# Optimization experiments

Hardware: AMD Instinct MI355X
Metric: run time of the kernel (lower is better)

The kernel has to match this reference:

```python
import jax, jax.numpy as jnp
import numpy as np

VOCAB, HIDDEN, EMBED = 30522, 768, 512
PAD_INDEX = 0
NEG_SLOPE = 0.1


def setup_inputs() -> dict:
    key = jax.random.key(0)
    k1, k2, k3, k4 = jax.random.split(key, 4)
    words = jax.random.randint(k1, (16, 512, 4), 0, VOCAB, dtype=jnp.int64) if jax.config.jax_enable_x64 else jax.random.randint(k1, (16, 512, 4), 0, VOCAB, dtype=jnp.int32)
    embed_table = jax.random.normal(k2, (VOCAB, HIDDEN), dtype=jnp.float32) * 0.02
    w_ffn = jax.random.normal(k3, (HIDDEN, EMBED), dtype=jnp.float32) * 0.02
    b_ffn = jax.random.normal(k4, (EMBED,), dtype=jnp.float32) * 0.02
    return {"words": words, "embed_table": embed_table, "w_ffn": w_ffn, "b_ffn": b_ffn}


def reference(words, embed_table, w_ffn, b_ffn):
    # words: [B, S, W] subword ids; pad_index marks padding subwords/words.
    B, S, W = words.shape
    sub_mask = words != PAD_INDEX                      # [B,S,W] valid subwords
    word_valid = jnp.any(sub_mask, axis=-1)            # [B,S]  words with >=1 subword
    lens = jnp.sum(word_valid, axis=-1)                # [B]    valid words per sequence

    # Stub of transformer last_hidden_state: per-token hidden vectors. [B,S,W,H]
    x = embed_table[words]

    # Masked mean over subwords of each word (segment mean-pool).
    m = sub_mask[..., None].astype(x.dtype)
    cnt = jnp.maximum(jnp.sum(sub_mask, axis=-1), 1)[..., None].astype(x.dtype)
    pooled = jnp.sum(x * m, axis=2) / cnt              # [B,S,H]

    # pad = x[0, -1] of flattened [B, S*W, H] == hidden of last flat token of batch 0
    pad_vec = x[0, -1, -1]                             # [H]

    # Stable compaction: valid words first (mirrors pop-in-order + pad append).
    order = jnp.argsort(jnp.logical_not(word_valid), axis=1, stable=True)  # [B,S]
    pooled_c = jnp.take_along_axis(pooled, order[..., None], axis=1)       # [B,S,H]
    keep = (jnp.arange(S)[None, :] < lens[:, None])[..., None]             # [B,S,1]
    x_seq = jnp.where(keep, pooled_c, pad_vec)         # [B,S,H]

    # FFN: Linear + LeakyReLU(0.1)
    return jax.nn.leaky_relu(x_seq @ w_ffn + b_ffn, NEG_SLOPE)
```

## Files before the change

### kernel.cpp

```cpp
#include <hip/hip_runtime.h>
#include <stdint.h>

#define HIDDEN 768
#define EMBED  512
#define BATCH  16
#define SEQ    512
#define NWORDS (BATCH*SEQ)
#define PAD_FLAT_IDX 2047
#define NEG_SLOPE 0.1f
#define NPOOLBLK 2048

__device__ __forceinline__ unsigned short f2bf(float f) {
    unsigned int x = __float_as_uint(f);
    unsigned int r = x + 0x7fffu + ((x >> 16) & 1u);
    return (unsigned short)(r >> 16);
}

__global__ __launch_bounds__(256) void combo_kernel(const int* __restrict__ words,
                                                    const float* __restrict__ w,
                                                    const float* __restrict__ table,
                                                    unsigned short* __restrict__ xseq,
                                                    unsigned short* __restrict__ wt) {
    if (blockIdx.x < NPOOLBLK) {
        __shared__ unsigned long long mask[8];
        int b    = blockIdx.x >> 7;
        int wave = threadIdx.x >> 6;
        int lane = threadIdx.x & 63;

        int p0 = wave * 64 + lane;
        int p1 = p0 + 256;
        int4 wa = ((const int4*)words)[b * SEQ + p0];
        int4 wb = ((const int4*)words)[b * SEQ + p1];
        unsigned long long mlo = __ballot((wa.x | wa.y | wa.z | wa.w) != 0);
        unsigned long long mhi = __ballot((wb.x | wb.y | wb.z | wb.w) != 0);
        if (lane == 0) { mask[wave] = mlo; mask[4 + wave] = mhi; }
        __syncthreads();

        int s = (blockIdx.x & 127) * 4 + wave;
        int seg = s >> 6;
        int bit = s & 63;
        int vp = 0, tot = 0;
#pragma unroll
        for (int i = 0; i < 8; ++i) {
            unsigned long long m = mask[i];
            int c = __popcll(m);
            if (i < seg) vp += c;
            tot += c;
        }
        unsigned long long mseg = mask[seg];
        vp += __popcll(mseg & ((1ull << bit) - 1ull));
        bool valid = (mseg >> bit) & 1ull;
        int d = valid ? vp : (tot + (s - vp));
        int drow = b * SEQ + d;

        int4 w4 = ((const int4*)words)[b * SEQ + s];
        int cnt = (w4.x != 0) + (w4.y != 0) + (w4.z != 0) + (w4.w != 0);

        float sx[3] = {0.f, 0.f, 0.f}, sy[3] = {0.f, 0.f, 0.f};
        float sz[3] = {0.f, 0.f, 0.f}, sw[3] = {0.f, 0.f, 0.f};
        if (cnt == 0) {
            int pid = words[PAD_FLAT_IDX];
            const float4* rp = (const float4*)(table + (size_t)pid * HIDDEN);
#pragma unroll
            for (int c = 0; c < 3; ++c) {
                float4 v = rp[lane + 64 * c];
                sx[c] = v.x; sy[c] = v.y; sz[c] = v.z; sw[c] = v.w;
            }
            cnt = 1;
        } else {
            int id[4] = {w4.x, w4.y, w4.z, w4.w};
#pragma unroll
            for (int j = 0; j < 4; ++j) {
                if (id[j] != 0) {
                    const float4* rp = (const float4*)(table + (size_t)id[j] * HIDDEN);
#pragma unroll
                    for (int c = 0; c < 3; ++c) {
                        float4 v = rp[lane + 64 * c];
                        sx[c] += v.x; sy[c] += v.y; sz[c] += v.z; sw[c] += v.w;
                    }
                }
            }
        }
        float inv = 1.0f / (float)cnt;
#pragma unroll
        for (int c = 0; c < 3; ++c) {
            ushort4 o;
            o.x = f2bf(sx[c] * inv); o.y = f2bf(sy[c] * inv);
            o.z = f2bf(sz[c] * inv); o.w = f2bf(sw[c] * inv);
            *(ushort4*)&xseq[(size_t)drow * HIDDEN + (lane + 64 * c) * 4] = o;
        }
    } else {
        __shared__ float tile[32][33];
        int bid = blockIdx.x - NPOOLBLK;
        int k0 = (bid % (HIDDEN / 32)) * 32;
        int n0 = (bid / (HIDDEN / 32)) * 32;
        int tc = threadIdx.x & 31;
        int tr = threadIdx.x >> 5;
#pragma unroll
        for (int i = 0; i < 4; ++i) {
            int r = tr + i * 8;
            tile[r][tc] = w[(size_t)(k0 + r) * EMBED + n0 + tc];
        }
        __syncthreads();
#pragma unroll
        for (int i = 0; i < 4; ++i) {
            int r = tr + i * 8;
            wt[(size_t)(n0 + r) * HIDDEN + k0 + tc] = f2bf(tile[tc][r]);
        }
    }
}

typedef __attribute__((ext_vector_type(8))) short bf16x8;
typedef __attribute__((ext_vector_type(4))) float f32x4;

__device__ __forceinline__ void load_lds16(const void* g, void* l) {
    __builtin_amdgcn_global_load_lds(
        (const __attribute__((address_space(1))) unsigned int*)g,
        (__attribute__((address_space(3))) unsigned int*)l,
        16, 0, 0);
}

#define BM 128
#define BN 64
#define BK 32
#define NSTEP (HIDDEN / BK)
#define NBUF 4

__global__ __launch_bounds__(256) void gemm_kernel(const unsigned short* __restrict__ A,
                                                   const unsigned short* __restrict__ Bt,
                                                   const float* __restrict__ bias,
                                                   float* __restrict__ out) {
    __shared__ unsigned short sA[NBUF][BM * BK];
    __shared__ unsigned short sB[NBUF][BN * BK];

    int tid = threadIdx.x;
    int bid = blockIdx.x;
    int swz = (bid & 7) * 64 + (bid >> 3);
    int m0  = (swz >> 3) * BM;
    int n0  = (swz & 7) * BN;
    int wave = tid >> 6;
    int lane = tid & 63;
    int wr   = wave >> 1;
    int wc   = wave & 1;
    int quad = lane >> 4;
    int l16  = lane & 15;

    f32x4 acc[4][2] = {};

    const unsigned short* ga0 = A  + (size_t)(m0 + (tid >> 2)) * HIDDEN + (tid & 3) * 8;
    const unsigned short* ga1 = A  + (size_t)(m0 + 64 + (tid >> 2)) * HIDDEN + (tid & 3) * 8;
    const unsigned short* gb  = Bt + (size_t)(n0 + (tid >> 2)) * HIDDEN + (tid & 3) * 8;

    load_lds16(ga0,      &sA[0][tid * 8]);
    load_lds16(ga1,      &sA[0][(256 + tid) * 8]);
    load_lds16(gb,       &sB[0][tid * 8]);
    load_lds16(ga0 + BK, &sA[1][tid * 8]);
    load_lds16(ga1 + BK, &sA[1][(256 + tid) * 8]);
    load_lds16(gb  + BK, &sB[1][tid * 8]);

#pragma unroll
    for (int t = 0; t < NSTEP; ++t) {
        if (t + 2 < NSTEP) {
            const int k0  = (t + 2) * BK;
            const int buf = (t + 2) & (NBUF - 1);
            load_lds16(ga0 + k0, &sA[buf][tid * 8]);
            load_lds16(ga1 + k0, &sA[buf][(256 + tid) * 8]);
            load_lds16(gb  + k0, &sB[buf][tid * 8]);
        }
        if (t < NSTEP - 2)
            asm volatile("s_waitcnt vmcnt(6)\n\ts_barrier" ::: "memory");
        else if (t == NSTEP - 2)
            asm volatile("s_waitcnt vmcnt(3)\n\ts_barrier" ::: "memory");
        else
            asm volatile("s_waitcnt vmcnt(0)\n\ts_barrier" ::: "memory");

        const int buf = t & (NBUF - 1);
        bf16x8 af[4], bfr[2];
#pragma unroll
        for (int mt = 0; mt < 4; ++mt)
            af[mt] = *(const bf16x8*)&sA[buf][(wr * 64 + mt * 16 + l16) * BK + quad * 8];
#pragma unroll
        for (int nt = 0; nt < 2; ++nt)
            bfr[nt] = *(const bf16x8*)&sB[buf][(wc * 32 + nt * 16 + l16) * BK + quad * 8];

#pragma unroll
        for (int mt = 0; mt < 4; ++mt)
#pragma unroll
            for (int nt = 0; nt < 2; ++nt)
                acc[mt][nt] = __builtin_amdgcn_mfma_f32_16x16x32_bf16(
                    af[mt], bfr[nt], acc[mt][nt], 0, 0, 0);
    }

#pragma unroll
    for (int nt = 0; nt < 2; ++nt) {
        int col = n0 + wc * 32 + nt * 16 + l16;
        float bv = bias[col];
#pragma unroll
        for (int mt = 0; mt < 4; ++mt) {
            int rbase = m0 + wr * 64 + mt * 16 + quad * 4;
#pragma unroll
            for (int r = 0; r < 4; ++r) {
                float v = acc[mt][nt][r] + bv;
                v = (v > 0.f) ? v : v * NEG_SLOPE;
                out[(size_t)(rbase + r) * EMBED + col] = v;
            }
        }
    }
}

extern "C" void kernel_launch(void* const* d_in, const int* in_sizes, int n_in,
                              void* d_out, int out_size, void* d_ws, size_t ws_size,
                              hipStream_t stream) {
    (void)in_sizes; (void)n_in; (void)out_size; (void)ws_size;
    const int*   words = (const int*)d_in[0];
    const float* table = (const float*)d_in[1];
    const float* wffn  = (const float*)d_in[2];
    const float* bffn  = (const float*)d_in[3];
    float* out = (float*)d_out;

    char* ws = (char*)d_ws;
    unsigned short* xseq = (unsigned short*)ws;
    unsigned short* wt   = (unsigned short*)(ws + 12582912);

    combo_kernel<<<NPOOLBLK + (HIDDEN / 32) * (EMBED / 32), 256, 0, stream>>>(
        words, wffn, table, xseq, wt);
    gemm_kernel<<<NWORDS / BM * (EMBED / BN), 256, 0, stream>>>(xseq, wt, bffn, out);
}
```

Baseline: 160.6 us.

## Fuse pooling, weight transpose and GEMM into one persistent kernel with grid barrier

```diff
diff --git a/kernel.cpp b/kernel.cpp
--- a/kernel.cpp
+++ b/kernel.cpp
@@ -8,7 +8,11 @@
 #define NWORDS (BATCH*SEQ)
 #define PAD_FLAT_IDX 2047
 #define NEG_SLOPE 0.1f
-#define NPOOLBLK 2048
+
+#define NBLK       512
+#define XSEQ_BYTES 12582912
+#define WT_BYTES   786432
+#define CTR_OFF    (XSEQ_BYTES + WT_BYTES)
 
 __device__ __forceinline__ unsigned short f2bf(float f) {
     unsigned int x = __float_as_uint(f);
@@ -16,19 +20,41 @@
     return (unsigned short)(r >> 16);
 }
 
-__global__ __launch_bounds__(256) void combo_kernel(const int* __restrict__ words,
-                                                    const float* __restrict__ w,
-                                                    const float* __restrict__ table,
-                                                    unsigned short* __restrict__ xseq,
-                                                    unsigned short* __restrict__ wt) {
-    if (blockIdx.x < NPOOLBLK) {
-        __shared__ unsigned long long mask[8];
-        int b    = blockIdx.x >> 7;
-        int wave = threadIdx.x >> 6;
-        int lane = threadIdx.x & 63;
-
-        int p0 = wave * 64 + lane;
-        int p1 = p0 + 256;
+typedef __attribute__((ext_vector_type(8))) short bf16x8;
+typedef __attribute__((ext_vector_type(4))) float f32x4;
+
+__device__ __forceinline__ void load_lds16(const void* g, void* l) {
+    __builtin_amdgcn_global_load_lds(
+        (const __attribute__((address_space(1))) unsigned int*)g,
+        (__attribute__((address_space(3))) unsigned int*)l,
+        16, 0, 0);
+}
+
+#define BM 128
+#define BN 64
+#define BK 32
+#define NSTEP (HIDDEN / BK)
+#define NBUF 4
+
+__global__ __launch_bounds__(256, 2) void fused_kernel(
+    const int* __restrict__ words, const float* __restrict__ w,
+    const float* __restrict__ table, const float* __restrict__ bias,
+    float* __restrict__ out, unsigned short* __restrict__ xseq,
+    unsigned short* __restrict__ wt, unsigned int* __restrict__ ctr)
+{
+    __shared__ unsigned short sA[NBUF][BM * BK];
+    __shared__ unsigned short sB[NBUF][BN * BK];
+    __shared__ unsigned long long mask[8];
+
+    int tid  = threadIdx.x;
+    int bid  = blockIdx.x;
+    int wave = tid >> 6;
+    int lane = tid & 63;
+
+    {
+        int b = bid >> 5;
+        int q = bid & 31;
+        int p0 = wave * 64 + lane, p1 = p0 + 256;
         int4 wa = ((const int4*)words)[b * SEQ + p0];
         int4 wb = ((const int4*)words)[b * SEQ + p1];
         unsigned long long mlo = __ballot((wa.x | wa.y | wa.z | wa.w) != 0);
@@ -36,66 +62,86 @@
         if (lane == 0) { mask[wave] = mlo; mask[4 + wave] = mhi; }
         __syncthreads();
 
-        int s = (blockIdx.x & 127) * 4 + wave;
-        int seg = s >> 6;
-        int bit = s & 63;
-        int vp = 0, tot = 0;
-#pragma unroll
-        for (int i = 0; i < 8; ++i) {
-            unsigned long long m = mask[i];
-            int c = __popcll(m);
-            if (i < seg) vp += c;
-            tot += c;
-        }
-        unsigned long long mseg = mask[seg];
-        vp += __popcll(mseg & ((1ull << bit) - 1ull));
-        bool valid = (mseg >> bit) & 1ull;
-        int d = valid ? vp : (tot + (s - vp));
-        int drow = b * SEQ + d;
-
-        int4 w4 = ((const int4*)words)[b * SEQ + s];
-        int cnt = (w4.x != 0) + (w4.y != 0) + (w4.z != 0) + (w4.w != 0);
-
-        float sx[3] = {0.f, 0.f, 0.f}, sy[3] = {0.f, 0.f, 0.f};
-        float sz[3] = {0.f, 0.f, 0.f}, sw[3] = {0.f, 0.f, 0.f};
-        if (cnt == 0) {
-            int pid = words[PAD_FLAT_IDX];
-            const float4* rp = (const float4*)(table + (size_t)pid * HIDDEN);
+        int s0 = q * 16 + wave * 4;
+        const int4* w4p = (const int4*)words + b * SEQ;
+        int4 wv[4] = { w4p[s0], w4p[s0 + 1], w4p[s0 + 2], w4p[s0 + 3] };
+
+        float4 g[2][12];
+#define PREFETCH(BUFI, V)                                                      \
+        {                                                                      \
+            const float4* r0 = (const float4*)(table + (size_t)(V).x * HIDDEN);\
+            const float4* r1 = (const float4*)(table + (size_t)(V).y * HIDDEN);\
+            const float4* r2 = (const float4*)(table + (size_t)(V).z * HIDDEN);\
+            const float4* r3 = (const float4*)(table + (size_t)(V).w * HIDDEN);\
+            g[BUFI][0] = r0[lane]; g[BUFI][1]  = r0[lane + 64]; g[BUFI][2]  = r0[lane + 128]; \
+            g[BUFI][3] = r1[lane]; g[BUFI][4]  = r1[lane + 64]; g[BUFI][5]  = r1[lane + 128]; \
+            g[BUFI][6] = r2[lane]; g[BUFI][7]  = r2[lane + 64]; g[BUFI][8]  = r2[lane + 128]; \
+            g[BUFI][9] = r3[lane]; g[BUFI][10] = r3[lane + 64]; g[BUFI][11] = r3[lane + 128]; \
+        }
+        PREFETCH(0, wv[0])
+#pragma unroll
+        for (int j = 0; j < 4; ++j) {
+            if (j < 3) {
+                if (((j + 1) & 1) == 0) PREFETCH(0, wv[j + 1])
+                else                    PREFETCH(1, wv[j + 1])
+            }
+            int s = s0 + j;
+            int seg = s >> 6, bit = s & 63;
+            int vp = 0, tot = 0;
+#pragma unroll
+            for (int i = 0; i < 8; ++i) {
+                unsigned long long m = mask[i];
+                int c = __popcll(m);
+                if (i < seg) vp += c;
+                tot += c;
+            }
+            unsigned long long mseg = mask[seg];
+            vp += __popcll(mseg & ((1ull << bit) - 1ull));
+            bool valid = (mseg >> bit) & 1ull;
+            int d = valid ? vp : (tot + (s - vp));
+            int drow = b * SEQ + d;
+
+            int4 v4 = wv[j];
+            int cnt = (v4.x != 0) + (v4.y != 0) + (v4.z != 0) + (v4.w != 0);
+            float sx[3] = {0.f,0.f,0.f}, sy[3] = {0.f,0.f,0.f};
+            float sz[3] = {0.f,0.f,0.f}, sw[3] = {0.f,0.f,0.f};
+            if (cnt == 0) {
+                int pid = words[PAD_FLAT_IDX];
+                const float4* rp = (const float4*)(table + (size_t)pid * HIDDEN);
+#pragma unroll
+                for (int c = 0; c < 3; ++c) {
+                    float4 v = rp[lane + 64 * c];
+                    sx[c] = v.x; sy[c] = v.y; sz[c] = v.z; sw[c] = v.w;
+                }
+                cnt = 1;
+            } else {
+                const float4* gg = (j & 1) ? g[1] : g[0];
+#pragma unroll
+                for (int c = 0; c < 3; ++c) {
+                    if (v4.x) { sx[c] += gg[0+c].x; sy[c] += gg[0+c].y; sz[c] += gg[0+c].z; sw[c] += gg[0+c].w; }
+                    if (v4.y) { sx[c] += gg[3+c].x; sy[c] += gg[3+c].y; sz[c] += gg[3+c].z; sw[c] += gg[3+c].w; }
+                    if (v4.z) { sx[c] += gg[6+c].x; sy[c] += gg[6+c].y; sz[c] += gg[6+c].z; sw[c] += gg[6+c].w; }
+                    if (v4.w) { sx[c] += gg[9+c].x; sy[c] += gg[9+c].y; sz[c] += gg[9+c].z; sw[c] += gg[9+c].w; }
+                }
+            }
+            float inv = 1.0f / (float)cnt;
 #pragma unroll
             for (int c = 0; c < 3; ++c) {
-                float4 v = rp[lane + 64 * c];
-                sx[c] = v.x; sy[c] = v.y; sz[c] = v.z; sw[c] = v.w;
-            }
-            cnt = 1;
-        } else {
-            int id[4] = {w4.x, w4.y, w4.z, w4.w};
-#pragma unroll
-            for (int j = 0; j < 4; ++j) {
-                if (id[j] != 0) {
-                    const float4* rp = (const float4*)(table + (size_t)id[j] * HIDDEN);
-#pragma unroll
-                    for (int c = 0; c < 3; ++c) {
-                        float4 v = rp[lane + 64 * c];
-                        sx[c] += v.x; sy[c] += v.y; sz[c] += v.z; sw[c] += v.w;
-                    }
-                }
-            }
-        }
-        float inv = 1.0f / (float)cnt;
-#pragma unroll
-        for (int c = 0; c < 3; ++c) {
-            ushort4 o;
-            o.x = f2bf(sx[c] * inv); o.y = f2bf(sy[c] * inv);
-            o.z = f2bf(sz[c] * inv); o.w = f2bf(sw[c] * inv);
-            *(ushort4*)&xseq[(size_t)drow * HIDDEN + (lane + 64 * c) * 4] = o;
-        }
-    } else {
-        __shared__ float tile[32][33];
-        int bid = blockIdx.x - NPOOLBLK;
+                ushort4 o;
+                o.x = f2bf(sx[c] * inv); o.y = f2bf(sy[c] * inv);
+                o.z = f2bf(sz[c] * inv); o.w = f2bf(sw[c] * inv);
+                *(ushort4*)&xseq[(size_t)drow * HIDDEN + (lane + 64 * c) * 4] = o;
+            }
+        }
+#undef PREFETCH
+    }
+
+    if (bid < 384) {
+        float (*tile)[33] = (float (*)[33])(&sA[0][0]);
         int k0 = (bid % (HIDDEN / 32)) * 32;
         int n0 = (bid / (HIDDEN / 32)) * 32;
-        int tc = threadIdx.x & 31;
-        int tr = threadIdx.x >> 5;
+        int tc = tid & 31;
+        int tr = tid >> 5;
 #pragma unroll
         for (int i = 0; i < 4; ++i) {
             int r = tr + i * 8;
@@ -108,101 +154,86 @@
             wt[(size_t)(n0 + r) * HIDDEN + k0 + tc] = f2bf(tile[tc][r]);
         }
     }
-}
-
-typedef __attribute__((ext_vector_type(8))) short bf16x8;
-typedef __attribute__((ext_vector_type(4))) float f32x4;
-
-__device__ __forceinline__ void load_lds16(const void* g, void* l) {
-    __builtin_amdgcn_global_load_lds(
-        (const __attribute__((address_space(1))) unsigned int*)g,
-        (__attribute__((address_space(3))) unsigned int*)l,
-        16, 0, 0);
-}
-
-#define BM 128
-#define BN 64
-#define BK 32
-#define NSTEP (HIDDEN / BK)
-#define NBUF 4
-
-__global__ __launch_bounds__(256) void gemm_kernel(const unsigned short* __restrict__ A,
-                                                   const unsigned short* __restrict__ Bt,
-                                                   const float* __restrict__ bias,
-                                                   float* __restrict__ out) {
-    __shared__ unsigned short sA[NBUF][BM * BK];
-    __shared__ unsigned short sB[NBUF][BN * BK];
-
-    int tid = threadIdx.x;
-    int bid = blockIdx.x;
-    int swz = (bid & 7) * 64 + (bid >> 3);
-    int m0  = (swz >> 3) * BM;
-    int n0  = (swz & 7) * BN;
-    int wave = tid >> 6;
-    int lane = tid & 63;
-    int wr   = wave >> 1;
-    int wc   = wave & 1;
-    int quad = lane >> 4;
-    int l16  = lane & 15;
-
-    f32x4 acc[4][2] = {};
-
-    const unsigned short* ga0 = A  + (size_t)(m0 + (tid >> 2)) * HIDDEN + (tid & 3) * 8;
-    const unsigned short* ga1 = A  + (size_t)(m0 + 64 + (tid >> 2)) * HIDDEN + (tid & 3) * 8;
-    const unsigned short* gb  = Bt + (size_t)(n0 + (tid >> 2)) * HIDDEN + (tid & 3) * 8;
-
-    load_lds16(ga0,      &sA[0][tid * 8]);
-    load_lds16(ga1,      &sA[0][(256 + tid) * 8]);
-    load_lds16(gb,       &sB[0][tid * 8]);
-    load_lds16(ga0 + BK, &sA[1][tid * 8]);
-    load_lds16(ga1 + BK, &sA[1][(256 + tid) * 8]);
-    load_lds16(gb  + BK, &sB[1][tid * 8]);
-
-#pragma unroll
-    for (int t = 0; t < NSTEP; ++t) {
-        if (t + 2 < NSTEP) {
-            const int k0  = (t + 2) * BK;
-            const int buf = (t + 2) & (NBUF - 1);
-            load_lds16(ga0 + k0, &sA[buf][tid * 8]);
-            load_lds16(ga1 + k0, &sA[buf][(256 + tid) * 8]);
-            load_lds16(gb  + k0, &sB[buf][tid * 8]);
-        }
-        if (t < NSTEP - 2)
-            asm volatile("s_waitcnt vmcnt(6)\n\ts_barrier" ::: "memory");
-        else if (t == NSTEP - 2)
-            asm volatile("s_waitcnt vmcnt(3)\n\ts_barrier" ::: "memory");
-        else
-            asm volatile("s_waitcnt vmcnt(0)\n\ts_barrier" ::: "memory");
-
-        const int buf = t & (NBUF - 1);
-        bf16x8 af[4], bfr[2];
-#pragma unroll
-        for (int mt = 0; mt < 4; ++mt)
-            af[mt] = *(const bf16x8*)&sA[buf][(wr * 64 + mt * 16 + l16) * BK + quad * 8];
-#pragma unroll
-        for (int nt = 0; nt < 2; ++nt)
-            bfr[nt] = *(const bf16x8*)&sB[buf][(wc * 32 + nt * 16 + l16) * BK + quad * 8];
-
-#pragma unroll
-        for (int mt = 0; mt < 4; ++mt)
+
+    __threadfence();
+    __syncthreads();
+    if (tid == 0) {
+        __hip_atomic_fetch_add(ctr, 1u, __ATOMIC_ACQ_REL, __HIP_MEMORY_SCOPE_AGENT);
+        long long spin = 0;
+        while (__hip_atomic_load(ctr, __ATOMIC_ACQUIRE, __HIP_MEMORY_SCOPE_AGENT) < NBLK) {
+            if (++spin > (1ll << 22)) break;
+        }
+    }
+    __syncthreads();
+
+    {
+        int swz = (bid & 7) * 64 + (bid >> 3);
+        int m0  = (swz >> 3) * BM;
+        int n0  = (swz & 7) * BN;
+        int wr  = wave >> 1;
+        int wc  = wave & 1;
+        int quad = lane >> 4;
+        int l16  = lane & 15;
+
+        f32x4 acc[4][2] = {};
+
+        const unsigned short* ga0 = xseq + (size_t)(m0 + (tid >> 2)) * HIDDEN + (tid & 3) * 8;
+        const unsigned short* ga1 = xseq + (size_t)(m0 + 64 + (tid >> 2)) * HIDDEN + (tid & 3) * 8;
+        const unsigned short* gb  = wt   + (size_t)(n0 + (tid >> 2)) * HIDDEN + (tid & 3) * 8;
+
+        load_lds16(ga0,      &sA[0][tid * 8]);
+        load_lds16(ga1,      &sA[0][(256 + tid) * 8]);
+        load_lds16(gb,       &sB[0][tid * 8]);
+        load_lds16(ga0 + BK, &sA[1][tid * 8]);
+        load_lds16(ga1 + BK, &sA[1][(256 + tid) * 8]);
+        load_lds16(gb  + BK, &sB[1][tid * 8]);
+
+#pragma unroll
+        for (int t = 0; t < NSTEP; ++t) {
+            if (t + 2 < NSTEP) {
+                const int k0  = (t + 2) * BK;
+                const int buf = (t + 2) & (NBUF - 1);
+                load_lds16(ga0 + k0, &sA[buf][tid * 8]);
+                load_lds16(ga1 + k0, &sA[buf][(256 + tid) * 8]);
+                load_lds16(gb  + k0, &sB[buf][tid * 8]);
+            }
+            if (t < NSTEP - 2)
+                asm volatile("s_waitcnt vmcnt(6)\n\ts_barrier" ::: "memory");
+            else if (t == NSTEP - 2)
+                asm volatile("s_waitcnt vmcnt(3)\n\ts_barrier" ::: "memory");
+            else
+                asm volatile("s_waitcnt vmcnt(0)\n\ts_barrier" ::: "memory");
+
+            const int buf = t & (NBUF - 1);
+            bf16x8 af[4], bfr[2];
+#pragma unroll
+            for (int mt = 0; mt < 4; ++mt)
+                af[mt] = *(const bf16x8*)&sA[buf][(wr * 64 + mt * 16 + l16) * BK + quad * 8];
 #pragma unroll
             for (int nt = 0; nt < 2; ++nt)
-                acc[mt][nt] = __builtin_amdgcn_mfma_f32_16x16x32_bf16(
-                    af[mt], bfr[nt], acc[mt][nt], 0, 0, 0);
-    }
-
-#pragma unroll
-    for (int nt = 0; nt < 2; ++nt) {
-        int col = n0 + wc * 32 + nt * 16 + l16;
-        float bv = bias[col];
-#pragma unroll
-        for (int mt = 0; mt < 4; ++mt) {
-            int rbase = m0 + wr * 64 + mt * 16 + quad * 4;
-#pragma unroll
-            for (int r = 0; r < 4; ++r) {
-                float v = acc[mt][nt][r] + bv;
-                v = (v > 0.f) ? v : v * NEG_SLOPE;
-                out[(size_t)(rbase + r) * EMBED + col] = v;
+                bfr[nt] = *(const bf16x8*)&sB[buf][(wc * 32 + nt * 16 + l16) * BK + quad * 8];
+
+#pragma unroll
+            for (int mt = 0; mt < 4; ++mt)
+#pragma unroll
+                for (int nt = 0; nt < 2; ++nt)
+                    acc[mt][nt] = __builtin_amdgcn_mfma_f32_16x16x32_bf16(
+                        af[mt], bfr[nt], acc[mt][nt], 0, 0, 0);
+        }
+
+#pragma unroll
+        for (int nt = 0; nt < 2; ++nt) {
+            int col = n0 + wc * 32 + nt * 16 + l16;
+            float bv = bias[col];
+#pragma unroll
+            for (int mt = 0; mt < 4; ++mt) {
+                int rbase = m0 + wr * 64 + mt * 16 + quad * 4;
+#pragma unroll
+                for (int r = 0; r < 4; ++r) {
+                    float v = acc[mt][nt][r] + bv;
+                    v = (v > 0.f) ? v : v * NEG_SLOPE;
+                    out[(size_t)(rbase + r) * EMBED + col] = v;
+                }
             }
         }
     }
@@ -220,9 +251,9 @@
 
     char* ws = (char*)d_ws;
     unsigned short* xseq = (unsigned short*)ws;
-    unsigned short* wt   = (unsigned short*)(ws + 12582912);
-
-    combo_kernel<<<NPOOLBLK + (HIDDEN / 32) * (EMBED / 32), 256, 0, stream>>>(
-        words, wffn, table, xseq, wt);
-    gemm_kernel<<<NWORDS / BM * (EMBED / BN), 256, 0, stream>>>(xseq, wt, bffn, out);
-}
+    unsigned short* wt   = (unsigned short*)(ws + XSEQ_BYTES);
+    unsigned int*   ctr  = (unsigned int*)(ws + CTR_OFF);
+
+    hipMemsetAsync(ctr, 0, 64, stream);
+    fused_kernel<<<NBLK, 256, 0, stream>>>(words, wffn, table, bffn, out, xseq, wt, ctr);
+}
```

Result: slower. 277.3 us (+72.6%).
